# Optimization experiments

Measured on AMD Instinct MI355X. Metric: run time of the kernel, lower is better.

The kernel has to match this reference:

```python
import jax, jax.numpy as jnp
import numpy as np

EMBED = 1024
N, L = 8, 1024


def setup_inputs() -> dict:
    key = jax.random.key(0)
    ks = jax.random.split(key, 6)
    return {
        "values": jax.random.normal(ks[0], (N, L, EMBED), dtype=jnp.float32),
        "keys": jax.random.normal(ks[1], (N, L, EMBED), dtype=jnp.float32),
        "query": jax.random.normal(ks[2], (N, L, EMBED), dtype=jnp.float32),
        "mask": jax.random.randint(ks[3], (N, 1, L, L), 0, 2, dtype=jnp.int32),
        "W_out": jax.random.normal(ks[4], (EMBED, EMBED), dtype=jnp.float32) * (EMBED ** -0.5),
        "b_out": jax.random.normal(ks[5], (EMBED,), dtype=jnp.float32) * 0.01,
        "heads": 16,
    }


def reference(values, keys, query, mask, W_out, b_out, heads):
    n, q_len, embed = query.shape
    k_len = keys.shape[1]
    v_len = values.shape[1]
    head_dim = embed // heads
    # split heads: (N, len, H, D)
    v = values.reshape(n, v_len, heads, head_dim)
    k = keys.reshape(n, k_len, heads, head_dim)
    q = query.reshape(n, q_len, heads, head_dim)
    # raw dot-product scores (note: the original module never applies its Q/K/V linears)
    energy = jnp.einsum('nqhd,nkhd->nhqk', q, k)  # (N, H, Q, K)
    # faithful quirk: masked positions set to +1e-20 (not -inf), BEFORE scaling
    energy = jnp.where(mask == 0, jnp.float32(1e-20), energy)
    # faithful quirk: scale by sqrt(embed_size), not sqrt(head_dim)
    attention = jax.nn.softmax(energy / jnp.sqrt(jnp.float32(embed)), axis=3)
    out = jnp.einsum('nhqk,nkhd->nqhd', attention, v).reshape(n, q_len, embed)
    # fc_out: torch Linear stores weight (out, in); y = x @ W^T + b
    return out @ W_out.T + b_out
```

## Files before the change

kernel.cpp:

```cpp
#include <hip/hip_runtime.h>
#include <hip/hip_bf16.h>

typedef __attribute__((ext_vector_type(8))) short bf16x8;
typedef __attribute__((ext_vector_type(4))) float f32x4;

#define SWZ(row, byteofs) (((row)*128) + ((byteofs) ^ (((row)&7)<<4)))

__device__ __forceinline__ unsigned pk2(float a, float b){
  __hip_bfloat162 h = __float22bfloat162_rn(make_float2(a, b));
  unsigned u; __builtin_memcpy(&u, &h, 4);
  return u;
}

__device__ __forceinline__ void gld16(const void* g, void* l){
  __builtin_amdgcn_global_load_lds((const __attribute__((address_space(1))) void*)g,
                                   (__attribute__((address_space(3))) void*)l, 16, 0, 0);
}

union bfpack { bf16x8 v; unsigned u[4]; uint4 q; };

__global__ __launch_bounds__(256) void mask_bits_kernel(const int* __restrict__ mask,
                                                        unsigned* __restrict__ bits){
  int t = blockIdx.x * 256 + threadIdx.x;
  int u = t >> 6;
  int lane = t & 63;
  int row = u >> 4;
  int chunk = u & 15;
  int m = mask[(size_t)row * 1024 + chunk * 64 + lane];
  unsigned long long b = __ballot(m != 0);
  if (lane == 0){
    unsigned* p = bits + row * 32 + chunk * 2;
    p[0] = (unsigned)(b & 0xffffffffull);
    p[1] = (unsigned)(b >> 32);
  }
}

__global__ __launch_bounds__(256) void wconv_kernel(const float* __restrict__ W,
                                                    unsigned short* __restrict__ Wb){
  int i = blockIdx.x * 256 + threadIdx.x;
  float4 f = reinterpret_cast<const float4*>(W)[i];
  uint2 o = make_uint2(pk2(f.x, f.y), pk2(f.z, f.w));
  reinterpret_cast<uint2*>(Wb)[i] = o;
}

__global__ __launch_bounds__(256) void permqk_kernel(const float* __restrict__ src,
                                                     unsigned short* __restrict__ dst){
  int w = blockIdx.x * 4 + (threadIdx.x >> 6);
  int lane = threadIdx.x & 63;
  int n = w >> 11, h = (w >> 7) & 15, l8 = w & 127;
  int l = l8 * 8 + (lane >> 3);
  int dch = (lane & 7) * 8;
  const float* sp = src + ((size_t)n * 1024 + l) * 1024 + h * 64 + dch;
  float4 a = *reinterpret_cast<const float4*>(sp);
  float4 b = *reinterpret_cast<const float4*>(sp + 4);
  uint4 o = make_uint4(pk2(a.x,a.y), pk2(a.z,a.w), pk2(b.x,b.y), pk2(b.z,b.w));
  *reinterpret_cast<uint4*>(dst + (((size_t)n * 16 + h) * 1024 + l) * 64 + dch) = o;
}

__global__ __launch_bounds__(256) void permv_kernel(const float* __restrict__ src,
                                                    unsigned short* __restrict__ dst){
  __shared__ __attribute__((aligned(16))) unsigned short T[64*64];
  int bid = blockIdx.x;
  int n = bid >> 8, h = (bid >> 4) & 15, l0 = (bid & 15) * 64;
  int t = threadIdx.x;
  {
    int l = t >> 2, dseg = t & 3;
    const float* sp = src + ((size_t)n * 1024 + l0 + l) * 1024 + h * 64 + dseg * 16;
    float4 f0 = *reinterpret_cast<const float4*>(sp + 0);
    float4 f1 = *reinterpret_cast<const float4*>(sp + 4);
    float4 f2 = *reinterpret_cast<const float4*>(sp + 8);
    float4 f3 = *reinterpret_cast<const float4*>(sp + 12);
    uint4 lo = make_uint4(pk2(f0.x,f0.y), pk2(f0.z,f0.w), pk2(f1.x,f1.y), pk2(f1.z,f1.w));
    uint4 hi = make_uint4(pk2(f2.x,f2.y), pk2(f2.z,f2.w), pk2(f3.x,f3.y), pk2(f3.z,f3.w));
    *reinterpret_cast<uint4*>((char*)T + SWZ(l, dseg*32))      = lo;
    *reinterpret_cast<uint4*>((char*)T + SWZ(l, dseg*32 + 16)) = hi;
  }
  __syncthreads();
  {
    int d = t >> 2, lseg = t & 3;
    for (int j = 0; j < 2; ++j){
      bf16x8 wv;
      #pragma unroll
      for (int i = 0; i < 8; ++i){
        int l = lseg*16 + j*8 + i;
        wv[i] = *(const short*)((const char*)T + (size_t)l*128 + ((d*2) ^ (i<<4)));
      }
      *reinterpret_cast<bf16x8*>(dst + (((size_t)n * 16 + h) * 64 + d) * 1024 + l0 + lseg*16 + j*8) = wv;
    }
  }
}

__global__ __launch_bounds__(256) void attn_kernel(
    const float* __restrict__ Q, const unsigned short* __restrict__ Kb,
    const unsigned short* __restrict__ Vtg, const unsigned* __restrict__ bits,
    unsigned short* __restrict__ Obf)
{
  __shared__ __attribute__((aligned(16))) unsigned short Kt[2][64*64];
  __shared__ __attribute__((aligned(16))) unsigned short Vt[2][64*64];
  __shared__ __attribute__((aligned(16))) unsigned short Pl[4][16*64];

  int bid = blockIdx.x;
  int wg = ((bid & 7) << 8) | (bid >> 3);
  int qb = wg & 15, h = (wg >> 4) & 15, n = wg >> 8;

  int tid = threadIdx.x, wid = tid >> 6, lane = tid & 63, lg = lane >> 4, lc = lane & 15;
  int qbase = qb * 64 + wid * 16;

  const unsigned short* Kh = Kb  + ((size_t)(n*16 + h)) * 1024 * 64;
  const unsigned short* Vh = Vtg + ((size_t)(n*16 + h)) * 64 * 1024;

  bf16x8 qf[2];
  {
    const float* qp = Q + (size_t)(n*1024 + qbase + lc) * 1024 + h*64;
    #pragma unroll
    for (int c = 0; c < 2; ++c){
      float4 a0 = *reinterpret_cast<const float4*>(qp + c*32 + lg*8);
      float4 a1 = *reinterpret_cast<const float4*>(qp + c*32 + lg*8 + 4);
      bfpack pk;
      pk.u[0] = pk2(a0.x,a0.y); pk.u[1] = pk2(a0.z,a0.w);
      pk.u[2] = pk2(a1.x,a1.y); pk.u[3] = pk2(a1.z,a1.w);
      qf[c] = pk.v;
    }
  }

  const int s0 = tid, s1 = tid + 256;
  const int r0 = s0 >> 3, c0 = ((s0 & 7) * 16) ^ ((r0 & 7) << 4);
  const int r1 = s1 >> 3, c1 = ((s1 & 7) * 16) ^ ((r1 & 7) << 4);

#define STAGE(KB, BUF) do { \
    gld16((const char*)Kh + ((size_t)((KB)*64 + r0) * 128 + c0), (char*)Kt[BUF] + s0*16); \
    gld16((const char*)Kh + ((size_t)((KB)*64 + r1) * 128 + c1), (char*)Kt[BUF] + s1*16); \
    gld16((const char*)Vh + ((size_t)r0 * 2048 + (KB)*128 + c0), (char*)Vt[BUF] + s0*16); \
    gld16((const char*)Vh + ((size_t)r1 * 2048 + (KB)*128 + c1), (char*)Vt[BUF] + s1*16); \
  } while(0)

  int pa[4];
  #pragma unroll
  for (int t = 0; t < 4; ++t)
    pa[t] = lc*128 + ((((t*16 + lg*4)*2)) ^ ((lc & 7) << 4));

  f32x4 acc[4];
  for (int i = 0; i < 4; ++i) acc[i] = (f32x4){0.f,0.f,0.f,0.f};
  float lsum = 0.f;
  const float c2 = 0.04508422002777998f;

  STAGE(0, 0);
  int cur = 0;

  for (int kb = 0; kb < 16; ++kb){
    __syncthreads();
    if (kb < 15) STAGE(kb + 1, cur ^ 1);

    uint2 mw = *reinterpret_cast<const uint2*>(bits + (size_t)(n*1024 + qbase + lc) * 32 + kb*2);
    unsigned ws0 = mw.x >> (lg*4);
    unsigned ws1 = mw.y >> (lg*4);

    f32x4 Sw[4];
    #pragma unroll
    for (int t = 0; t < 4; ++t) Sw[t] = (f32x4){0.f,0.f,0.f,0.f};
    __builtin_amdgcn_s_setprio(1);
    #pragma unroll
    for (int t = 0; t < 4; ++t)
      #pragma unroll
      for (int c = 0; c < 2; ++c){
        bf16x8 kf = *reinterpret_cast<const bf16x8*>((const char*)Kt[cur] + SWZ(t*16 + lc, lg*16 + c*64));
        Sw[t] = __builtin_amdgcn_mfma_f32_16x16x32_bf16(kf, qf[c], Sw[t], 0, 0, 0);
      }
    __builtin_amdgcn_s_setprio(0);

    unsigned short* pl = &Pl[wid][0];
    #pragma unroll
    for (int t = 0; t < 4; ++t){
      unsigned w = (t >= 2) ? ws1 : ws0;
      float p0 = ((w >> ((t&1)*16 + 0)) & 1u) ? exp2f(Sw[t][0]*c2) : 1.0f;
      float p1 = ((w >> ((t&1)*16 + 1)) & 1u) ? exp2f(Sw[t][1]*c2) : 1.0f;
      float p2 = ((w >> ((t&1)*16 + 2)) & 1u) ? exp2f(Sw[t][2]*c2) : 1.0f;
      float p3 = ((w >> ((t&1)*16 + 3)) & 1u) ? exp2f(Sw[t][3]*c2) : 1.0f;
      lsum += (p0 + p1) + (p2 + p3);
      uint2 pw = make_uint2(pk2(p0, p1), pk2(p2, p3));
      *reinterpret_cast<uint2*>((char*)pl + pa[t]) = pw;
    }

    __builtin_amdgcn_s_setprio(1);
    #pragma unroll
    for (int kc = 0; kc < 2; ++kc){
      bf16x8 af = *reinterpret_cast<const bf16x8*>((const char*)pl + SWZ(lc, lg*16 + kc*64));
      #pragma unroll
      for (int t2 = 0; t2 < 4; ++t2){
        bf16x8 vf = *reinterpret_cast<const bf16x8*>((const char*)Vt[cur] + SWZ(t2*16 + lc, lg*16 + kc*64));
        acc[t2] = __builtin_amdgcn_mfma_f32_16x16x32_bf16(af, vf, acc[t2], 0, 0, 0);
      }
    }
    __builtin_amdgcn_s_setprio(0);
    cur ^= 1;
  }
#undef STAGE

  lsum += __shfl_xor(lsum, 16, 64);
  lsum += __shfl_xor(lsum, 32, 64);

  #pragma unroll
  for (int r = 0; r < 4; ++r){
    float tot = __shfl(lsum, lg*4 + r, 16);
    float inv = 1.0f / tot;
    size_t qg = (size_t)(n*1024 + qbase + lg*4 + r);
    unsigned short* op = Obf + (qg * 16 + h) * 64;
    unsigned w01 = pk2(acc[0][r]*inv, acc[1][r]*inv);
    unsigned w23 = pk2(acc[2][r]*inv, acc[3][r]*inv);
    op[0*16 + lc] = (unsigned short)w01;
    op[1*16 + lc] = (unsigned short)(w01 >> 16);
    op[2*16 + lc] = (unsigned short)w23;
    op[3*16 + lc] = (unsigned short)(w23 >> 16);
  }
}

__global__ __launch_bounds__(256) void out_gemm_kernel(
    const unsigned short* __restrict__ A, const unsigned short* __restrict__ B,
    const float* __restrict__ bias, float* __restrict__ out)
{
  __shared__ __attribute__((aligned(16))) unsigned short As[2][128*64];
  __shared__ __attribute__((aligned(16))) unsigned short Bs[2][128*64];

  int mb = blockIdx.x;
  int nb = blockIdx.y;
  int tid = threadIdx.x, wid = tid >> 6, lane = tid & 63, lg = lane >> 4, lc = lane & 15;
  int wr = wid >> 1, wc = wid & 1;

  int rr[4], cc[4];
  #pragma unroll
  for (int i = 0; i < 4; ++i){
    int s = tid + 256*i;
    rr[i] = s >> 3;
    cc[i] = ((s & 7) * 16) ^ ((rr[i] & 7) << 4);
  }

#define GSTAGE(KB, BUF) do { \
    _Pragma("unroll") \
    for (int i = 0; i < 4; ++i){ \
      int s = tid + 256*i; \
      gld16((const char*)A + ((size_t)(mb*128 + rr[i]) * 1024 + (KB)*64) * 2 + cc[i], (char*)As[BUF] + s*16); \
      gld16((const char*)B + ((size_t)(nb*128 + rr[i]) * 1024 + (KB)*64) * 2 + cc[i], (char*)Bs[BUF] + s*16); \
    } \
  } while(0)

  f32x4 acc[4][4];
  for (int m = 0; m < 4; ++m)
    for (int nn2 = 0; nn2 < 4; ++nn2) acc[m][nn2] = (f32x4){0.f,0.f,0.f,0.f};

  GSTAGE(0, 0);
  int cur = 0;

  for (int kb = 0; kb < 16; ++kb){
    __syncthreads();
    if (kb < 15) GSTAGE(kb + 1, cur ^ 1);
    #pragma unroll
    for (int kc = 0; kc < 2; ++kc){
      bf16x8 af[4], bfr[4];
      #pragma unroll
      for (int m = 0; m < 4; ++m)
        af[m] = *reinterpret_cast<const bf16x8*>((const char*)As[cur] + SWZ(wr*64 + m*16 + lc, kc*64 + lg*16));
      #pragma unroll
      for (int nn2 = 0; nn2 < 4; ++nn2)
        bfr[nn2] = *reinterpret_cast<const bf16x8*>((const char*)Bs[cur] + SWZ(wc*64 + nn2*16 + lc, kc*64 + lg*16));
      __builtin_amdgcn_s_setprio(1);
      #pragma unroll
      for (int m = 0; m < 4; ++m)
        #pragma unroll
        for (int nn2 = 0; nn2 < 4; ++nn2)
          acc[m][nn2] = __builtin_amdgcn_mfma_f32_16x16x32_bf16(af[m], bfr[nn2], acc[m][nn2], 0, 0, 0);
      __builtin_amdgcn_s_setprio(0);
    }
    cur ^= 1;
  }
#undef GSTAGE

  for (int nn2 = 0; nn2 < 4; ++nn2){
    int col = nb*128 + wc*64 + nn2*16 + lc;
    float bv = bias[col];
    for (int m = 0; m < 4; ++m){
      int rowb = mb*128 + wr*64 + m*16 + lg*4;
      for (int r = 0; r < 4; ++r)
        out[(size_t)(rowb + r) * 1024 + col] = acc[m][nn2][r] + bv;
    }
  }
}

extern "C" void kernel_launch(void* const* d_in, const int* in_sizes, int n_in,
                              void* d_out, int out_size, void* d_ws, size_t ws_size,
                              hipStream_t stream) {
  const float* V  = (const float*)d_in[0];
  const float* K  = (const float*)d_in[1];
  const float* Q  = (const float*)d_in[2];
  const int* mask = (const int*)d_in[3];
  const float* W  = (const float*)d_in[4];
  const float* b  = (const float*)d_in[5];
  float* out = (float*)d_out;

  char* ws = (char*)d_ws;
  unsigned* bits       = (unsigned*)ws;
  unsigned short* Wb   = (unsigned short*)(ws + (1u<<20));
  unsigned short* Obf  = (unsigned short*)(ws + (3u<<20));
  unsigned short* Vtg  = (unsigned short*)(ws + (19u<<20));
  unsigned short* Kb   = (unsigned short*)d_out;

  mask_bits_kernel<<<32768, 256, 0, stream>>>(mask, bits);
  wconv_kernel<<<1024, 256, 0, stream>>>(W, Wb);
  permqk_kernel<<<4096, 256, 0, stream>>>(K, Kb);
  permv_kernel<<<2048, 256, 0, stream>>>(V, Vtg);
  attn_kernel<<<2048, 256, 0, stream>>>(Q, Kb, Vtg, bits, Obf);
  dim3 g(64, 8);
  out_gemm_kernel<<<g, 256, 0, stream>>>(Obf, Wb, b, out);
}
```

Before: 139.4 us.

## Rewrite softmax as masked (exp-1) plus precomputed V column sums in fp16

Every masked score contributes exp(~0)=1, so the kernel now seeds the output accumulator with per-head column sums of V, which permv_kernel computes as it transposes. Inside the loop it only adds (exp2(s)-1) for unmasked entries. The exponent now runs as packed fp16 h2exp2, the mask is pre-expanded to bytes and applied with a byte-permute AND, and P·V switches to fp16 MFMA. The row sum comes from an extra MFMA against a ones vector, plus 1024. This removes the per-element branches and the scalar exp work, but adds reads of a byte mask eight times larger than the bit mask, one extra MFMA per chunk, and fp16 range and precision risk.

```diff
diff --git a/kernel.cpp b/kernel.cpp
--- a/kernel.cpp
+++ b/kernel.cpp
@@ -1,7 +1,9 @@
 #include <hip/hip_runtime.h>
 #include <hip/hip_bf16.h>
+#include <hip/hip_fp16.h>
 
 typedef __attribute__((ext_vector_type(8))) short bf16x8;
+typedef __attribute__((ext_vector_type(8))) _Float16 f16x8;
 typedef __attribute__((ext_vector_type(4))) float f32x4;
 
 #define SWZ(row, byteofs) (((row)*128) + ((byteofs) ^ (((row)&7)<<4)))
@@ -12,6 +14,12 @@
   return u;
 }
 
+__device__ __forceinline__ unsigned pkh(float a, float b){
+  auto h = __builtin_amdgcn_cvt_pkrtz(a, b);
+  unsigned u; __builtin_memcpy(&u, &h, 4);
+  return u;
+}
+
 __device__ __forceinline__ void gld16(const void* g, void* l){
   __builtin_amdgcn_global_load_lds((const __attribute__((address_space(1))) void*)g,
                                    (__attribute__((address_space(3))) void*)l, 16, 0, 0);
@@ -19,20 +27,17 @@
 
 union bfpack { bf16x8 v; unsigned u[4]; uint4 q; };
 
-__global__ __launch_bounds__(256) void mask_bits_kernel(const int* __restrict__ mask,
-                                                        unsigned* __restrict__ bits){
-  int t = blockIdx.x * 256 + threadIdx.x;
-  int u = t >> 6;
-  int lane = t & 63;
-  int row = u >> 4;
-  int chunk = u & 15;
-  int m = mask[(size_t)row * 1024 + chunk * 64 + lane];
-  unsigned long long b = __ballot(m != 0);
-  if (lane == 0){
-    unsigned* p = bits + row * 32 + chunk * 2;
-    p[0] = (unsigned)(b & 0xffffffffull);
-    p[1] = (unsigned)(b >> 32);
-  }
+__global__ __launch_bounds__(256) void maskex_kernel(const int* __restrict__ mask,
+                                                     unsigned* __restrict__ mex){
+  size_t i = (size_t)blockIdx.x * 256 + threadIdx.x;
+  const int4* mp = reinterpret_cast<const int4*>(mask) + i * 4;
+  int4 a = mp[0], b = mp[1], c = mp[2], d = mp[3];
+  uint4 o;
+  o.x = (a.x?0xFFu:0u)|(a.y?0xFF00u:0u)|(a.z?0xFF0000u:0u)|(a.w?0xFF000000u:0u);
+  o.y = (b.x?0xFFu:0u)|(b.y?0xFF00u:0u)|(b.z?0xFF0000u:0u)|(b.w?0xFF000000u:0u);
+  o.z = (c.x?0xFFu:0u)|(c.y?0xFF00u:0u)|(c.z?0xFF0000u:0u)|(c.w?0xFF000000u:0u);
+  o.w = (d.x?0xFFu:0u)|(d.y?0xFF00u:0u)|(d.z?0xFF0000u:0u)|(d.w?0xFF000000u:0u);
+  reinterpret_cast<uint4*>(mex)[i] = o;
 }
 
 __global__ __launch_bounds__(256) void wconv_kernel(const float* __restrict__ W,
@@ -58,10 +63,12 @@
 }
 
 __global__ __launch_bounds__(256) void permv_kernel(const float* __restrict__ src,
-                                                    unsigned short* __restrict__ dst){
+                                                    unsigned short* __restrict__ dst,
+                                                    float* __restrict__ Vpart){
   __shared__ __attribute__((aligned(16))) unsigned short T[64*64];
+  __shared__ float red[256];
   int bid = blockIdx.x;
-  int n = bid >> 8, h = (bid >> 4) & 15, l0 = (bid & 15) * 64;
+  int n = bid >> 8, h = (bid >> 4) & 15, lt = bid & 15, l0 = lt * 64;
   int t = threadIdx.x;
   {
     int l = t >> 2, dseg = t & 3;
@@ -70,14 +77,15 @@
     float4 f1 = *reinterpret_cast<const float4*>(sp + 4);
     float4 f2 = *reinterpret_cast<const float4*>(sp + 8);
     float4 f3 = *reinterpret_cast<const float4*>(sp + 12);
-    uint4 lo = make_uint4(pk2(f0.x,f0.y), pk2(f0.z,f0.w), pk2(f1.x,f1.y), pk2(f1.z,f1.w));
-    uint4 hi = make_uint4(pk2(f2.x,f2.y), pk2(f2.z,f2.w), pk2(f3.x,f3.y), pk2(f3.z,f3.w));
+    uint4 lo = make_uint4(pkh(f0.x,f0.y), pkh(f0.z,f0.w), pkh(f1.x,f1.y), pkh(f1.z,f1.w));
+    uint4 hi = make_uint4(pkh(f2.x,f2.y), pkh(f2.z,f2.w), pkh(f3.x,f3.y), pkh(f3.z,f3.w));
     *reinterpret_cast<uint4*>((char*)T + SWZ(l, dseg*32))      = lo;
     *reinterpret_cast<uint4*>((char*)T + SWZ(l, dseg*32 + 16)) = hi;
   }
   __syncthreads();
   {
     int d = t >> 2, lseg = t & 3;
+    float s = 0.f;
     for (int j = 0; j < 2; ++j){
       bf16x8 wv;
       #pragma unroll
@@ -86,14 +94,25 @@
         wv[i] = *(const short*)((const char*)T + (size_t)l*128 + ((d*2) ^ (i<<4)));
       }
       *reinterpret_cast<bf16x8*>(dst + (((size_t)n * 16 + h) * 64 + d) * 1024 + l0 + lseg*16 + j*8) = wv;
-    }
+      #pragma unroll
+      for (int i = 0; i < 8; i += 2){
+        unsigned u = (unsigned)(unsigned short)wv[i] | ((unsigned)(unsigned short)wv[i+1] << 16);
+        __half2 hh; __builtin_memcpy(&hh, &u, 4);
+        float2 f = __half22float2(hh);
+        s += f.x + f.y;
+      }
+    }
+    red[t] = s;
+    __syncthreads();
+    if (lseg == 0)
+      Vpart[((size_t)(n*16 + h)*64 + d)*16 + lt] = red[t] + red[t+1] + red[t+2] + red[t+3];
   }
 }
 
 __global__ __launch_bounds__(256) void attn_kernel(
     const float* __restrict__ Q, const unsigned short* __restrict__ Kb,
-    const unsigned short* __restrict__ Vtg, const unsigned* __restrict__ bits,
-    unsigned short* __restrict__ Obf)
+    const unsigned short* __restrict__ Vtg, const unsigned char* __restrict__ Mex8,
+    const float* __restrict__ Vpart, unsigned short* __restrict__ Obf)
 {
   __shared__ __attribute__((aligned(16))) unsigned short Kt[2][64*64];
   __shared__ __attribute__((aligned(16))) unsigned short Vt[2][64*64];
@@ -108,6 +127,7 @@
 
   const unsigned short* Kh = Kb  + ((size_t)(n*16 + h)) * 1024 * 64;
   const unsigned short* Vh = Vtg + ((size_t)(n*16 + h)) * 64 * 1024;
+  const char* m8 = (const char*)Mex8 + ((size_t)(n*1024 + qbase + lc)) * 1024;
 
   bf16x8 qf[2];
   {
@@ -139,10 +159,23 @@
   for (int t = 0; t < 4; ++t)
     pa[t] = lc*128 + ((((t*16 + lg*4)*2)) ^ ((lc & 7) << 4));
 
-  f32x4 acc[4];
-  for (int i = 0; i < 4; ++i) acc[i] = (f32x4){0.f,0.f,0.f,0.f};
-  float lsum = 0.f;
-  const float c2 = 0.04508422002777998f;
+  f32x4 acc[4], accd = (f32x4){0.f,0.f,0.f,0.f};
+  {
+    const float* vp0 = Vpart + (size_t)(n*16 + h) * 64 * 16;
+    #pragma unroll
+    for (int t2 = 0; t2 < 4; ++t2){
+      const float4* pp = reinterpret_cast<const float4*>(vp0 + (t2*16 + lc)*16);
+      float4 s0v = pp[0], s1v = pp[1], s2v = pp[2], s3v = pp[3];
+      float v = ((s0v.x+s0v.y)+(s0v.z+s0v.w)) + ((s1v.x+s1v.y)+(s1v.z+s1v.w))
+              + ((s2v.x+s2v.y)+(s2v.z+s2v.w)) + ((s3v.x+s3v.y)+(s3v.z+s3v.w));
+      acc[t2] = (f32x4){v,v,v,v};
+    }
+  }
+
+  const float c2 = 0.045084220027780106f;
+  const __half2 hone2 = __floats2half2_rn(1.f, 1.f);
+  const f16x8 onesf = {(_Float16)1.f,(_Float16)1.f,(_Float16)1.f,(_Float16)1.f,
+                       (_Float16)1.f,(_Float16)1.f,(_Float16)1.f,(_Float16)1.f};
 
   STAGE(0, 0);
   int cur = 0;
@@ -151,9 +184,10 @@
     __syncthreads();
     if (kb < 15) STAGE(kb + 1, cur ^ 1);
 
-    uint2 mw = *reinterpret_cast<const uint2*>(bits + (size_t)(n*1024 + qbase + lc) * 32 + kb*2);
-    unsigned ws0 = mw.x >> (lg*4);
-    unsigned ws1 = mw.y >> (lg*4);
+    unsigned msk[4];
+    #pragma unroll
+    for (int t = 0; t < 4; ++t)
+      msk[t] = *reinterpret_cast<const unsigned*>(m8 + kb*64 + t*16 + lg*4);
 
     f32x4 Sw[4];
     #pragma unroll
@@ -171,24 +205,27 @@
     unsigned short* pl = &Pl[wid][0];
     #pragma unroll
     for (int t = 0; t < 4; ++t){
-      unsigned w = (t >= 2) ? ws1 : ws0;
-      float p0 = ((w >> ((t&1)*16 + 0)) & 1u) ? exp2f(Sw[t][0]*c2) : 1.0f;
-      float p1 = ((w >> ((t&1)*16 + 1)) & 1u) ? exp2f(Sw[t][1]*c2) : 1.0f;
-      float p2 = ((w >> ((t&1)*16 + 2)) & 1u) ? exp2f(Sw[t][2]*c2) : 1.0f;
-      float p3 = ((w >> ((t&1)*16 + 3)) & 1u) ? exp2f(Sw[t][3]*c2) : 1.0f;
-      lsum += (p0 + p1) + (p2 + p3);
-      uint2 pw = make_uint2(pk2(p0, p1), pk2(p2, p3));
-      *reinterpret_cast<uint2*>((char*)pl + pa[t]) = pw;
+      unsigned u01 = pkh(Sw[t][0]*c2, Sw[t][1]*c2);
+      unsigned u23 = pkh(Sw[t][2]*c2, Sw[t][3]*c2);
+      __half2 h01, h23;
+      __builtin_memcpy(&h01, &u01, 4); __builtin_memcpy(&h23, &u23, 4);
+      h01 = __hsub2(h2exp2(h01), hone2);
+      h23 = __hsub2(h2exp2(h23), hone2);
+      __builtin_memcpy(&u01, &h01, 4); __builtin_memcpy(&u23, &h23, 4);
+      u01 &= __builtin_amdgcn_perm(0u, msk[t], 0x01010000u);
+      u23 &= __builtin_amdgcn_perm(0u, msk[t], 0x03030202u);
+      *reinterpret_cast<uint2*>((char*)pl + pa[t]) = make_uint2(u01, u23);
     }
 
     __builtin_amdgcn_s_setprio(1);
     #pragma unroll
     for (int kc = 0; kc < 2; ++kc){
-      bf16x8 af = *reinterpret_cast<const bf16x8*>((const char*)pl + SWZ(lc, lg*16 + kc*64));
+      f16x8 af = *reinterpret_cast<const f16x8*>((const char*)pl + SWZ(lc, lg*16 + kc*64));
+      accd = __builtin_amdgcn_mfma_f32_16x16x32_f16(af, onesf, accd, 0, 0, 0);
       #pragma unroll
       for (int t2 = 0; t2 < 4; ++t2){
-        bf16x8 vf = *reinterpret_cast<const bf16x8*>((const char*)Vt[cur] + SWZ(t2*16 + lc, lg*16 + kc*64));
-        acc[t2] = __builtin_amdgcn_mfma_f32_16x16x32_bf16(af, vf, acc[t2], 0, 0, 0);
+        f16x8 vf = *reinterpret_cast<const f16x8*>((const char*)Vt[cur] + SWZ(t2*16 + lc, lg*16 + kc*64));
+        acc[t2] = __builtin_amdgcn_mfma_f32_16x16x32_f16(af, vf, acc[t2], 0, 0, 0);
       }
     }
     __builtin_amdgcn_s_setprio(0);
@@ -196,13 +233,9 @@
   }
 #undef STAGE
 
-  lsum += __shfl_xor(lsum, 16, 64);
-  lsum += __shfl_xor(lsum, 32, 64);
-
   #pragma unroll
   for (int r = 0; r < 4; ++r){
-    float tot = __shfl(lsum, lg*4 + r, 16);
-    float inv = 1.0f / tot;
+    float inv = 1.0f / (1024.0f + accd[r]);
     size_t qg = (size_t)(n*1024 + qbase + lg*4 + r);
     unsigned short* op = Obf + (qg * 16 + h) * 64;
     unsigned w01 = pk2(acc[0][r]*inv, acc[1][r]*inv);
@@ -297,17 +330,18 @@
   float* out = (float*)d_out;
 
   char* ws = (char*)d_ws;
-  unsigned* bits       = (unsigned*)ws;
-  unsigned short* Wb   = (unsigned short*)(ws + (1u<<20));
-  unsigned short* Obf  = (unsigned short*)(ws + (3u<<20));
-  unsigned short* Vtg  = (unsigned short*)(ws + (19u<<20));
-  unsigned short* Kb   = (unsigned short*)d_out;
-
-  mask_bits_kernel<<<32768, 256, 0, stream>>>(mask, bits);
+  unsigned short* Wb    = (unsigned short*)ws;
+  unsigned short* Obf   = (unsigned short*)(ws + (2u<<20));
+  unsigned char*  Mex8  = (unsigned char*)(ws + (19u<<20));
+  float*          Vpart = (float*)(ws + (28u<<20));
+  unsigned short* Kb  = (unsigned short*)d_out;
+  unsigned short* Vtg = Kb + (size_t)8*1024*1024;
+
+  maskex_kernel<<<2048, 256, 0, stream>>>(mask, (unsigned*)Mex8);
   wconv_kernel<<<1024, 256, 0, stream>>>(W, Wb);
   permqk_kernel<<<4096, 256, 0, stream>>>(K, Kb);
-  permv_kernel<<<2048, 256, 0, stream>>>(V, Vtg);
-  attn_kernel<<<2048, 256, 0, stream>>>(Q, Kb, Vtg, bits, Obf);
+  permv_kernel<<<2048, 256, 0, stream>>>(V, Vtg, Vpart);
+  attn_kernel<<<2048, 256, 0, stream>>>(Q, Kb, Vtg, Mex8, Vpart, Obf);
   dim3 g(64, 8);
   out_gemm_kernel<<<g, 256, 0, stream>>>(Obf, Wb, b, out);
 }
```

Result: slower. 153.7 us (+10.2%).

## Use byte-mask expansion, branchless bf16 select, and MFMA row-sum for softmax denominator

Applied to the files above, without the earlier changes.

Replaces the ballot-based mask bitpacking kernel with a vectorized kernel that expands each mask int to a byte (0x00/0xFF). The attention kernel loads these bytes and uses v_perm to build 16-bit select masks that merge the bf16 exp values with bf16 ones without branching. It also computes the softmax denominator with an extra MFMA against a ones vector instead of scalar adds and shuffles, so the sum comes from the same rounded bf16 values used for P·V. The byte mask is 8x larger than the bit mask, so attention reads more mask bytes per tile, and the V transpose buffer now lives in the output buffer.

```diff
diff --git a/kernel.cpp b/kernel.cpp
--- a/kernel.cpp
+++ b/kernel.cpp
@@ -19,20 +19,17 @@
 
 union bfpack { bf16x8 v; unsigned u[4]; uint4 q; };
 
-__global__ __launch_bounds__(256) void mask_bits_kernel(const int* __restrict__ mask,
-                                                        unsigned* __restrict__ bits){
-  int t = blockIdx.x * 256 + threadIdx.x;
-  int u = t >> 6;
-  int lane = t & 63;
-  int row = u >> 4;
-  int chunk = u & 15;
-  int m = mask[(size_t)row * 1024 + chunk * 64 + lane];
-  unsigned long long b = __ballot(m != 0);
-  if (lane == 0){
-    unsigned* p = bits + row * 32 + chunk * 2;
-    p[0] = (unsigned)(b & 0xffffffffull);
-    p[1] = (unsigned)(b >> 32);
-  }
+__global__ __launch_bounds__(256) void maskex_kernel(const int* __restrict__ mask,
+                                                     unsigned* __restrict__ mex){
+  size_t i = (size_t)blockIdx.x * 256 + threadIdx.x;
+  const int4* mp = reinterpret_cast<const int4*>(mask) + i * 4;
+  int4 a = mp[0], b = mp[1], c = mp[2], d = mp[3];
+  uint4 o;
+  o.x = (a.x?0xFFu:0u)|(a.y?0xFF00u:0u)|(a.z?0xFF0000u:0u)|(a.w?0xFF000000u:0u);
+  o.y = (b.x?0xFFu:0u)|(b.y?0xFF00u:0u)|(b.z?0xFF0000u:0u)|(b.w?0xFF000000u:0u);
+  o.z = (c.x?0xFFu:0u)|(c.y?0xFF00u:0u)|(c.z?0xFF0000u:0u)|(c.w?0xFF000000u:0u);
+  o.w = (d.x?0xFFu:0u)|(d.y?0xFF00u:0u)|(d.z?0xFF0000u:0u)|(d.w?0xFF000000u:0u);
+  reinterpret_cast<uint4*>(mex)[i] = o;
 }
 
 __global__ __launch_bounds__(256) void wconv_kernel(const float* __restrict__ W,
@@ -92,7 +89,7 @@
 
 __global__ __launch_bounds__(256) void attn_kernel(
     const float* __restrict__ Q, const unsigned short* __restrict__ Kb,
-    const unsigned short* __restrict__ Vtg, const unsigned* __restrict__ bits,
+    const unsigned short* __restrict__ Vtg, const unsigned char* __restrict__ Mex8,
     unsigned short* __restrict__ Obf)
 {
   __shared__ __attribute__((aligned(16))) unsigned short Kt[2][64*64];
@@ -108,6 +105,7 @@
 
   const unsigned short* Kh = Kb  + ((size_t)(n*16 + h)) * 1024 * 64;
   const unsigned short* Vh = Vtg + ((size_t)(n*16 + h)) * 64 * 1024;
+  const char* m8 = (const char*)Mex8 + ((size_t)(n*1024 + qbase + lc)) * 1024;
 
   bf16x8 qf[2];
   {
@@ -139,10 +137,12 @@
   for (int t = 0; t < 4; ++t)
     pa[t] = lc*128 + ((((t*16 + lg*4)*2)) ^ ((lc & 7) << 4));
 
-  f32x4 acc[4];
+  f32x4 acc[4], accd = (f32x4){0.f,0.f,0.f,0.f};
   for (int i = 0; i < 4; ++i) acc[i] = (f32x4){0.f,0.f,0.f,0.f};
-  float lsum = 0.f;
-  const float c2 = 0.04508422002777998f;
+  const float scale = 0.03125f;
+  const unsigned ones2 = 0x3F803F80u;
+  const bf16x8 onesb = {(short)0x3F80,(short)0x3F80,(short)0x3F80,(short)0x3F80,
+                        (short)0x3F80,(short)0x3F80,(short)0x3F80,(short)0x3F80};
 
   STAGE(0, 0);
   int cur = 0;
@@ -151,9 +151,10 @@
     __syncthreads();
     if (kb < 15) STAGE(kb + 1, cur ^ 1);
 
-    uint2 mw = *reinterpret_cast<const uint2*>(bits + (size_t)(n*1024 + qbase + lc) * 32 + kb*2);
-    unsigned ws0 = mw.x >> (lg*4);
-    unsigned ws1 = mw.y >> (lg*4);
+    unsigned msk[4];
+    #pragma unroll
+    for (int t = 0; t < 4; ++t)
+      msk[t] = *reinterpret_cast<const unsigned*>(m8 + kb*64 + t*16 + lg*4);
 
     f32x4 Sw[4];
     #pragma unroll
@@ -171,20 +172,24 @@
     unsigned short* pl = &Pl[wid][0];
     #pragma unroll
     for (int t = 0; t < 4; ++t){
-      unsigned w = (t >= 2) ? ws1 : ws0;
-      float p0 = ((w >> ((t&1)*16 + 0)) & 1u) ? exp2f(Sw[t][0]*c2) : 1.0f;
-      float p1 = ((w >> ((t&1)*16 + 1)) & 1u) ? exp2f(Sw[t][1]*c2) : 1.0f;
-      float p2 = ((w >> ((t&1)*16 + 2)) & 1u) ? exp2f(Sw[t][2]*c2) : 1.0f;
-      float p3 = ((w >> ((t&1)*16 + 3)) & 1u) ? exp2f(Sw[t][3]*c2) : 1.0f;
-      lsum += (p0 + p1) + (p2 + p3);
-      uint2 pw = make_uint2(pk2(p0, p1), pk2(p2, p3));
-      *reinterpret_cast<uint2*>((char*)pl + pa[t]) = pw;
+      float e0 = __expf(Sw[t][0] * scale);
+      float e1 = __expf(Sw[t][1] * scale);
+      float e2 = __expf(Sw[t][2] * scale);
+      float e3 = __expf(Sw[t][3] * scale);
+      unsigned u01 = pk2(e0, e1);
+      unsigned u23 = pk2(e2, e3);
+      unsigned m01 = __builtin_amdgcn_perm(0u, msk[t], 0x01010000u);
+      unsigned m23 = __builtin_amdgcn_perm(0u, msk[t], 0x03030202u);
+      u01 = (u01 & m01) | (ones2 & ~m01);
+      u23 = (u23 & m23) | (ones2 & ~m23);
+      *reinterpret_cast<uint2*>((char*)pl + pa[t]) = make_uint2(u01, u23);
     }
 
     __builtin_amdgcn_s_setprio(1);
     #pragma unroll
     for (int kc = 0; kc < 2; ++kc){
       bf16x8 af = *reinterpret_cast<const bf16x8*>((const char*)pl + SWZ(lc, lg*16 + kc*64));
+      accd = __builtin_amdgcn_mfma_f32_16x16x32_bf16(af, onesb, accd, 0, 0, 0);
       #pragma unroll
       for (int t2 = 0; t2 < 4; ++t2){
         bf16x8 vf = *reinterpret_cast<const bf16x8*>((const char*)Vt[cur] + SWZ(t2*16 + lc, lg*16 + kc*64));
@@ -196,13 +201,9 @@
   }
 #undef STAGE
 
-  lsum += __shfl_xor(lsum, 16, 64);
-  lsum += __shfl_xor(lsum, 32, 64);
-
   #pragma unroll
   for (int r = 0; r < 4; ++r){
-    float tot = __shfl(lsum, lg*4 + r, 16);
-    float inv = 1.0f / tot;
+    float inv = 1.0f / accd[r];
     size_t qg = (size_t)(n*1024 + qbase + lg*4 + r);
     unsigned short* op = Obf + (qg * 16 + h) * 64;
     unsigned w01 = pk2(acc[0][r]*inv, acc[1][r]*inv);
@@ -297,17 +298,17 @@
   float* out = (float*)d_out;
 
   char* ws = (char*)d_ws;
-  unsigned* bits       = (unsigned*)ws;
-  unsigned short* Wb   = (unsigned short*)(ws + (1u<<20));
-  unsigned short* Obf  = (unsigned short*)(ws + (3u<<20));
-  unsigned short* Vtg  = (unsigned short*)(ws + (19u<<20));
-  unsigned short* Kb   = (unsigned short*)d_out;
-
-  mask_bits_kernel<<<32768, 256, 0, stream>>>(mask, bits);
+  unsigned char*  Mex8 = (unsigned char*)ws;
+  unsigned short* Wb   = (unsigned short*)(ws + (9u<<20));
+  unsigned short* Obf  = (unsigned short*)(ws + (11u<<20));
+  unsigned short* Kb  = (unsigned short*)d_out;
+  unsigned short* Vtg = Kb + (size_t)8*1024*1024;
+
+  maskex_kernel<<<2048, 256, 0, stream>>>(mask, (unsigned*)Mex8);
   wconv_kernel<<<1024, 256, 0, stream>>>(W, Wb);
   permqk_kernel<<<4096, 256, 0, stream>>>(K, Kb);
   permv_kernel<<<2048, 256, 0, stream>>>(V, Vtg);
-  attn_kernel<<<2048, 256, 0, stream>>>(Q, Kb, Vtg, bits, Obf);
+  attn_kernel<<<2048, 256, 0, stream>>>(Q, Kb, Vtg, Mex8, Obf);
   dim3 g(64, 8);
   out_gemm_kernel<<<g, 256, 0, stream>>>(Obf, Wb, b, out);
 }
```

After: 138.6 us. No clear change (-0.6%).
